# Kernel tuning notes

Hardware: AMD Instinct MI355X
Metric: run time of the kernel (lower is better)

The kernel has to match this reference:

```python
import jax, jax.numpy as jnp
import numpy as np
from jax.ops import segment_sum, segment_max

N_NODES = 100000
N_EDGES = 1600000
F_DIM = 64
N_GRAPHS = 64
K_HOPS = 3
EPS = 1e-5


def setup_inputs() -> dict:
    key = jax.random.key(0)
    ks = jax.random.split(key, 8)
    x = jax.random.normal(ks[0], (N_NODES, F_DIM), dtype=jnp.float32)
    edge_index = jax.random.randint(ks[1], (2, N_EDGES), 0, N_NODES, dtype=jnp.int32)
    batch = jnp.sort(jax.random.randint(ks[2], (N_NODES,), 0, N_GRAPHS, dtype=jnp.int32))
    edge_weight = jax.random.uniform(ks[3], (N_EDGES,), dtype=jnp.float32)
    # TAGConv params: K+1 hop-wise linear weights (no per-lin bias) + one output bias
    W = jax.random.normal(ks[4], (K_HOPS + 1, F_DIM, F_DIM), dtype=jnp.float32) * 0.05
    b = jnp.zeros((F_DIM,), dtype=jnp.float32)
    # GraphNorm params
    gn_weight = jnp.ones((F_DIM,), dtype=jnp.float32)
    gn_bias = jnp.zeros((F_DIM,), dtype=jnp.float32)
    gn_mean_scale = jnp.ones((F_DIM,), dtype=jnp.float32)
    return {"x": x, "edge_index": edge_index, "batch": batch, "edge_weight": edge_weight,
            "W": W, "b": b, "gn_weight": gn_weight, "gn_bias": gn_bias,
            "gn_mean_scale": gn_mean_scale}


def reference(x, edge_index, batch, edge_weight, W, b, gn_weight, gn_bias, gn_mean_scale):
    src, dst = edge_index[0], edge_index[1]

    # --- TAGConv: gcn_norm without self-loops ---
    deg = segment_sum(edge_weight, dst, num_segments=N_NODES)            # [N]
    dis = jnp.where(deg > 0, jax.lax.rsqrt(deg), 0.0)                    # deg^{-1/2}, inf -> 0
    norm = dis[src] * edge_weight * dis[dst]                             # [E]

    # out = sum_k (A_norm^k x) W_k + b
    out = x @ W[0]
    h = x
    for k in range(1, K_HOPS + 1):
        h = segment_sum(norm[:, None] * h[src], dst, num_segments=N_NODES)  # [N, F]
        out = out + h @ W[k]
    out = out + b

    # --- GraphNorm: per-graph mean/var with learnable mean_scale ---
    cnt = segment_sum(jnp.ones((N_NODES,), out.dtype), batch, num_segments=N_GRAPHS)
    cnt = jnp.maximum(cnt, 1.0)[:, None]                                  # [G, 1]
    mean = segment_sum(out, batch, num_segments=N_GRAPHS) / cnt          # [G, F]
    centered = out - mean[batch] * gn_mean_scale                         # [N, F]
    var = segment_sum(centered * centered, batch, num_segments=N_GRAPHS) / cnt
    hn = gn_weight * centered / jnp.sqrt(var + EPS)[batch] + gn_bias

    # --- residual + ReLU (add_residue=True) ---
    h_emb = jax.nn.relu(hn + x)                                          # [N, F]

    # --- global mean + max pooling ---
    mean_pool = segment_sum(h_emb, batch, num_segments=N_GRAPHS) / cnt   # [G, F]
    max_pool = segment_max(h_emb, batch, num_segments=N_GRAPHS)          # [G, F]
    flat = jnp.concatenate([mean_pool, max_pool], axis=-1)               # [G, 2F]

    return (h_emb, flat)
```

## Files before the change

kernel.cpp:

```cpp
#include <hip/hip_runtime.h>
#include <hip/hip_bf16.h>

#define NN 100000
#define NE 1600000
#define NG 64
#define FD 64
#define EPSV 1e-5f

typedef __hip_bfloat16 bf16;
typedef __attribute__((ext_vector_type(8))) short bf16x8;
typedef __attribute__((ext_vector_type(4))) float f32x4;

__device__ __forceinline__ float ldb(bf16 v) { return __bfloat162float(v); }
__device__ __forceinline__ bf16 f2b(float v) { return __float2bfloat16(v); }
__device__ __forceinline__ float b2f_bits(short s) {
    return __uint_as_float(((unsigned)(unsigned short)s) << 16);
}

#define NB1 391
#define CB 625
#define EPB 2560
#define CCN (NB1 * CB)
#define SCB2 ((CCN + 2047) / 2048)

__device__ __forceinline__ int xcd_chunk(int bid, int nwg) {
    int q = nwg >> 3, r = nwg & 7;
    int xcd = bid & 7, j = bid >> 3;
    return (xcd < r ? xcd * (q + 1) : r * (q + 1) + (xcd - r) * q) + j;
}

constexpr size_t ALGN(size_t x) { return (x + 255) & ~(size_t)255; }
constexpr size_t OFF_GSUM = 0;
constexpr size_t OFF_GSSQ = OFF_GSUM + ALGN((size_t)NG * FD * 4);
constexpr size_t OFF_GCNT = OFF_GSSQ + ALGN((size_t)NG * FD * 4);
constexpr size_t OFF_PSUM = OFF_GCNT + ALGN((size_t)NG * 4);
constexpr size_t OFF_PMAX = OFF_PSUM + ALGN((size_t)NG * FD * 4);
constexpr size_t ZERO_BYTES = OFF_PMAX + ALGN((size_t)NG * FD * 4);
constexpr size_t OFF_CNT  = ZERO_BYTES;
constexpr size_t OFF_DIS  = OFF_CNT  + ALGN((size_t)NN * 4);
constexpr size_t OFF_ROWP = OFF_DIS  + ALGN((size_t)NN * 4);
constexpr size_t OFF_BSUM = OFF_ROWP + ALGN((size_t)NN * 4);
constexpr size_t OFF_WT   = OFF_BSUM + ALGN(256 * 4);
constexpr size_t OFF_CSR  = OFF_WT   + ALGN(16384 * 2);
constexpr size_t OFF_H    = OFF_CSR  + ALGN((size_t)NE * 8);
constexpr size_t OFF_OUT  = OFF_H    + ALGN((size_t)NN * 256 * 2);
constexpr size_t OFF_CSRT = OFF_OUT;
constexpr size_t OFF_CC   = OFF_CSRT + ALGN((size_t)NE * 8);
static_assert(OFF_CC + (size_t)CCN * 4 - OFF_OUT <= (size_t)NN * FD * 4, "alias overflow");

#define XCB 25000
__global__ __launch_bounds__(256) void coarse_fused_kernel(const int* __restrict__ dst,
                                                           int* __restrict__ cc,
                                                           const float* __restrict__ x,
                                                           bf16* __restrict__ H,
                                                           const float* __restrict__ W,
                                                           bf16* __restrict__ Wt) {
    int b = blockIdx.x;
    if (b < CB) {
        __shared__ int hist[NB1];
        for (int i = threadIdx.x; i < NB1; i += 256) hist[i] = 0;
        __syncthreads();
        int e0 = b * EPB + threadIdx.x;
        #pragma unroll
        for (int i = 0; i < EPB / 256; i++)
            atomicAdd(&hist[dst[e0 + i * 256] >> 8], 1);
        __syncthreads();
        for (int i = threadIdx.x; i < NB1; i += 256)
            cc[(size_t)i * CB + b] = hist[i];
    } else if (b < CB + XCB) {
        int i = (b - CB) * 256 + threadIdx.x;
        if (i >= NN * 64) return;
        int node = i >> 6, f = i & 63;
        H[(size_t)node * 256 + f] = f2b(x[(size_t)node * 64 + f]);
    } else {
        int i = (b - CB - XCB) * 256 + threadIdx.x;
        int n = i & 63, kk = i >> 6;
        Wt[n * 256 + kk] = f2b(W[kk * 64 + n]);
    }
}

#define SCAN_BLK 256
#define SCAN_ITEMS 8
__global__ __launch_bounds__(SCAN_BLK) void scan_blocks(int* __restrict__ data,
                                                        int* __restrict__ bsum, int n) {
    __shared__ int lds[SCAN_BLK];
    int t = threadIdx.x, b = blockIdx.x;
    int base = b * SCAN_BLK * SCAN_ITEMS + t * SCAN_ITEMS;
    int v[SCAN_ITEMS];
    int s = 0;
    #pragma unroll
    for (int i = 0; i < SCAN_ITEMS; i++) {
        int idx = base + i;
        v[i] = (idx < n) ? data[idx] : 0;
        s += v[i];
    }
    lds[t] = s;
    __syncthreads();
    for (int off = 1; off < SCAN_BLK; off <<= 1) {
        int x = (t >= off) ? lds[t - off] : 0;
        __syncthreads();
        lds[t] += x;
        __syncthreads();
    }
    int excl = lds[t] - s;
    if (t == SCAN_BLK - 1) bsum[b] = lds[t];
    int run = excl;
    #pragma unroll
    for (int i = 0; i < SCAN_ITEMS; i++) {
        int idx = base + i;
        if (idx < n) data[idx] = run;
        run += v[i];
    }
}

__global__ __launch_bounds__(256) void bsum_scan(int* __restrict__ bsum, int nb) {
    __shared__ int lds[256];
    int t = threadIdx.x;
    int v = (t < nb) ? bsum[t] : 0;
    lds[t] = v;
    __syncthreads();
    for (int off = 1; off < 256; off <<= 1) {
        int x = (t >= off) ? lds[t - off] : 0;
        __syncthreads();
        lds[t] += x;
        __syncthreads();
    }
    if (t < nb) bsum[t] = lds[t] - v;
}

__global__ __launch_bounds__(256) void scan_add2(int* __restrict__ data,
                                                 const int* __restrict__ bpref, int n) {
    int i = blockIdx.x * 256 + threadIdx.x;
    if (i >= n) return;
    data[i] += bpref[i >> 11];
}

__global__ __launch_bounds__(256) void scatter2_kernel(const int* __restrict__ src,
                                                       const int* __restrict__ dst,
                                                       const float* __restrict__ ew,
                                                       const int* __restrict__ cc,
                                                       int2* __restrict__ csrt) {
    __shared__ int sc[512];
    __shared__ int gdel[NB1];
    __shared__ int2 stage[EPB];
    __shared__ int sdel[EPB];
    int t = threadIdx.x;
    int L = xcd_chunk(blockIdx.x, CB);

    sc[t] = 0; sc[t + 256] = 0;
    __syncthreads();

    int br[EPB / 256], px[EPB / 256], pw[EPB / 256];
    #pragma unroll
    for (int i = 0; i < EPB / 256; i++) {
        int e = L * EPB + i * 256 + t;
        int d = dst[e];
        int bk = d >> 8;
        int rk = atomicAdd(&sc[bk], 1);
        br[i] = bk | (rk << 9);
        px[i] = src[e] | ((d & 255) << 17);
        pw[i] = __float_as_int(ew[e]);
    }
    __syncthreads();

    for (int off = 1; off < 512; off <<= 1) {
        int a0 = (t >= off) ? sc[t - off] : 0;
        int a1 = sc[t + 256 - off];
        __syncthreads();
        sc[t] += a0; sc[t + 256] += a1;
        __syncthreads();
    }

    for (int i = t; i < NB1; i += 256)
        gdel[i] = cc[(size_t)i * CB + L] - ((i > 0) ? sc[i - 1] : 0);
    __syncthreads();

    #pragma unroll
    for (int i = 0; i < EPB / 256; i++) {
        int bk = br[i] & 511;
        int rk = br[i] >> 9;
        int slot = ((bk > 0) ? sc[bk - 1] : 0) + rk;
        stage[slot] = make_int2(px[i], pw[i]);
        sdel[slot] = gdel[bk];
    }
    __syncthreads();

    for (int j = t; j < EPB; j += 256)
        csrt[(size_t)(sdel[j] + j)] = stage[j];
}

__global__ __launch_bounds__(256) void fine_kernel(const int* __restrict__ cc,
                                                   const int2* __restrict__ csrt,
                                                   int2* __restrict__ csr,
                                                   int* __restrict__ rowp,
                                                   int* __restrict__ cnts,
                                                   float* __restrict__ dis) {
    __shared__ int hist[256];
    __shared__ float degw[256];
    __shared__ int pref[256];
    __shared__ int fcur[256];
    int b = blockIdx.x;
    int t = threadIdx.x;
    int base = cc[(size_t)b * CB];
    int end = (b == NB1 - 1) ? NE : cc[(size_t)(b + 1) * CB];
    int cnt = end - base;
    hist[t] = 0; degw[t] = 0.f;
    __syncthreads();
    for (int j = t; j < cnt; j += 256) {
        int2 e = csrt[base + j];
        int f = e.x >> 17;
        atomicAdd(&hist[f], 1);
        atomicAdd(&degw[f], __int_as_float(e.y));
    }
    __syncthreads();
    int hv = hist[t];
    pref[t] = hv;
    __syncthreads();
    for (int off = 1; off < 256; off <<= 1) {
        int x = (t >= off) ? pref[t - off] : 0;
        __syncthreads();
        pref[t] += x;
        __syncthreads();
    }
    int ex = pref[t] - hv;
    fcur[t] = ex;
    int node = b * 256 + t;
    if (node < NN) {
        rowp[node] = base + ex;
        cnts[node] = hv;
        float s = degw[t];
        dis[node] = (s > 0.f) ? rsqrtf(s) : 0.f;
    }
    __syncthreads();
    for (int j = t; j < cnt; j += 256) {
        int2 e = csrt[base + j];
        int f = e.x >> 17;
        int pos = atomicAdd(&fcur[f], 1);
        csr[base + pos] = make_int2(e.x & 0x1FFFF, e.y);
    }
}

template <bool FIRST>
__global__ __launch_bounds__(256) void hop_kernel(const bf16* __restrict__ hin,
                                                  bf16* __restrict__ hout,
                                                  const int* __restrict__ rowp,
                                                  const int* __restrict__ cnts,
                                                  int2* __restrict__ csr,
                                                  const float* __restrict__ dis) {
    int row = blockIdx.x * 4 + (threadIdx.x >> 6);
    if (row >= NN) return;
    row = __builtin_amdgcn_readfirstlane(row);
    int lane = threadIdx.x & 63;
    int sub = lane >> 3;
    int fl = lane & 7;
    int start = rowp[row];
    int cnt = cnts[row];
    float dr = dis[row];
    int2* cp = csr + start;

    float a[8] = {0, 0, 0, 0, 0, 0, 0, 0};

    if (cnt <= 24) {
        int2 e0 = (sub < cnt) ? cp[sub] : make_int2(0, 0);
        int2 e1 = (8 + sub < cnt) ? cp[8 + sub] : make_int2(0, 0);
        int2 e2 = (16 + sub < cnt) ? cp[16 + sub] : make_int2(0, 0);
        bf16x8 v0 = *(const bf16x8*)(hin + (size_t)e0.x * 256 + fl * 8);
        bf16x8 v1 = *(const bf16x8*)(hin + (size_t)e1.x * 256 + fl * 8);
        bf16x8 v2 = *(const bf16x8*)(hin + (size_t)e2.x * 256 + fl * 8);
        float w0 = __int_as_float(e0.y);
        float w1 = __int_as_float(e1.y);
        float w2 = __int_as_float(e2.y);
        if (FIRST) {
            w0 *= dis[e0.x]; w1 *= dis[e1.x]; w2 *= dis[e2.x];
            if (fl == 0) {
                if (sub < cnt)      cp[sub].y      = __float_as_int(w0);
                if (8 + sub < cnt)  cp[8 + sub].y  = __float_as_int(w1);
                if (16 + sub < cnt) cp[16 + sub].y = __float_as_int(w2);
            }
        }
        #pragma unroll
        for (int i = 0; i < 8; i++)
            a[i] = w0 * b2f_bits(v0[i]) + w1 * b2f_bits(v1[i]) + w2 * b2f_bits(v2[i]);
    } else {
        float b[8] = {0, 0, 0, 0, 0, 0, 0, 0};
        int j = 0;
        for (; j + 16 <= cnt; j += 16) {
            int2 e0 = cp[j + sub];
            int2 e1 = cp[j + 8 + sub];
            bf16x8 v0 = *(const bf16x8*)(hin + (size_t)e0.x * 256 + fl * 8);
            bf16x8 v1 = *(const bf16x8*)(hin + (size_t)e1.x * 256 + fl * 8);
            float w0 = __int_as_float(e0.y);
            float w1 = __int_as_float(e1.y);
            if (FIRST) {
                w0 *= dis[e0.x]; w1 *= dis[e1.x];
                if (fl == 0) {
                    cp[j + sub].y     = __float_as_int(w0);
                    cp[j + 8 + sub].y = __float_as_int(w1);
                }
            }
            #pragma unroll
            for (int i = 0; i < 8; i++) a[i] += w0 * b2f_bits(v0[i]);
            #pragma unroll
            for (int i = 0; i < 8; i++) b[i] += w1 * b2f_bits(v1[i]);
        }
        for (; j < cnt; j += 8) {
            int jj = j + sub;
            int2 e = (jj < cnt) ? cp[jj] : make_int2(0, 0);
            bf16x8 v = *(const bf16x8*)(hin + (size_t)e.x * 256 + fl * 8);
            float w = __int_as_float(e.y);
            if (FIRST) {
                w *= dis[e.x];
                if (fl == 0 && jj < cnt) cp[jj].y = __float_as_int(w);
            }
            #pragma unroll
            for (int i = 0; i < 8; i++) a[i] += w * b2f_bits(v[i]);
        }
        #pragma unroll
        for (int i = 0; i < 8; i++) a[i] += b[i];
    }

    #pragma unroll
    for (int i = 0; i < 8; i++) a[i] += __shfl_xor(a[i], 8);
    #pragma unroll
    for (int i = 0; i < 8; i++) a[i] += __shfl_xor(a[i], 16);
    #pragma unroll
    for (int i = 0; i < 8; i++) a[i] += __shfl_xor(a[i], 32);

    if (sub == 0) {
        bf16x8 ov;
        #pragma unroll
        for (int i = 0; i < 8; i++) {
            bf16 t = f2b(a[i] * dr);
            ov[i] = *(short*)&t;
        }
        *(bf16x8*)(hout + (size_t)row * 256 + fl * 8) = ov;
    }
}

#define GWAVES 1024
#define NT (NN / 16)

__global__ __launch_bounds__(256, 1) void gemm_kernel(const bf16* __restrict__ H,
                                                      const bf16* __restrict__ Wt,
                                                      const float* __restrict__ bias,
                                                      float* __restrict__ outb) {
    int wave = threadIdx.x >> 6;
    int lane = threadIdx.x & 63;
    int m = lane & 15, q = lane >> 4;
    int w = blockIdx.x * 4 + wave;

    bf16x8 B[4][8];
    #pragma unroll
    for (int n = 0; n < 4; n++) {
        const bf16* brow = Wt + (size_t)(n * 16 + m) * 256 + q * 8;
        #pragma unroll
        for (int ks = 0; ks < 8; ks++) B[n][ks] = *(const bf16x8*)(brow + ks * 32);
    }
    float bv[4];
    #pragma unroll
    for (int n = 0; n < 4; n++) bv[n] = bias[n * 16 + m];

    if (w >= NT) return;

    bf16x8 A0[8], A1[8];

    #define LOADA(dst_, t_)                                                  \
        {                                                                    \
            const bf16* arow = H + (size_t)((t_)*16 + m) * 256 + q * 8;      \
            _Pragma("unroll")                                                \
            for (int ks = 0; ks < 8; ks++)                                   \
                dst_[ks] = *(const bf16x8*)(arow + ks * 32);                 \
        }

    #define COMP(src_, t_)                                                   \
        {                                                                    \
            _Pragma("unroll")                                                \
            for (int n = 0; n < 4; n++) {                                    \
                f32x4 acc = {0.f, 0.f, 0.f, 0.f};                            \
                _Pragma("unroll")                                            \
                for (int ks = 0; ks < 8; ks++)                               \
                    acc = __builtin_amdgcn_mfma_f32_16x16x32_bf16(           \
                        src_[ks], B[n][ks], acc, 0, 0, 0);                   \
                _Pragma("unroll")                                            \
                for (int r = 0; r < 4; r++)                                  \
                    outb[(size_t)((t_)*16 + q * 4 + r) * 64 + n * 16 + m] =  \
                        acc[r] + bv[n];                                      \
            }                                                                \
        }

    int t = w;
    LOADA(A0, t)
    while (true) {
        int t1 = t + GWAVES;
        if (t1 < NT) LOADA(A1, t1)
        COMP(A0, t)
        if (t1 >= NT) return;
        int t2 = t1 + GWAVES;
        if (t2 < NT) LOADA(A0, t2)
        COMP(A1, t1)
        if (t2 >= NT) return;
        t = t2;
    }
    #undef LOADA
    #undef COMP
}

#define CH 32
#define STAT_WAVES ((NN + CH - 1) / CH)
#define STAT_BLOCKS ((STAT_WAVES * 64 + 255) / 256)

__global__ __launch_bounds__(256) void stats_kernel(const float* __restrict__ outb,
                                                    const int* __restrict__ batch,
                                                    float* __restrict__ gsum,
                                                    float* __restrict__ gssq,
                                                    float* __restrict__ gcnt) {
    int wid = (blockIdx.x * 256 + threadIdx.x) >> 6;
    int lane = threadIdx.x & 63;
    int n0 = wid * CH;
    if (n0 >= NN) return;
    int n1 = min(n0 + CH, NN);
    int g0 = batch[n0];
    if (n1 == n0 + CH && batch[n1 - 1] == g0) {
        float s = 0.f, s2 = 0.f;
        #pragma unroll
        for (int i = 0; i < CH; i++) {
            float v = outb[(size_t)(n0 + i) * 64 + lane];
            s += v; s2 += v * v;
        }
        atomicAdd(&gsum[g0 * 64 + lane], s);
        atomicAdd(&gssq[g0 * 64 + lane], s2);
        if (lane == 0) atomicAdd(&gcnt[g0], (float)CH);
    } else {
        int cur = g0; float s = 0.f, s2 = 0.f; int cl = 0;
        for (int i = n0; i < n1; i++) {
            int g = batch[i];
            if (g != cur) {
                atomicAdd(&gsum[cur * 64 + lane], s);
                atomicAdd(&gssq[cur * 64 + lane], s2);
                if (lane == 0) atomicAdd(&gcnt[cur], (float)cl);
                s = 0.f; s2 = 0.f; cl = 0; cur = g;
            }
            float v = outb[(size_t)i * 64 + lane];
            s += v; s2 += v * v; cl++;
        }
        atomicAdd(&gsum[cur * 64 + lane], s);
        atomicAdd(&gssq[cur * 64 + lane], s2);
        if (lane == 0) atomicAdd(&gcnt[cur], (float)cl);
    }
}

__device__ __forceinline__ void graph_mr(const float* gsum, const float* gssq,
                                         const float* gcnt, int g, int lane, float ms,
                                         float& mm, float& r) {
    float c = fmaxf(gcnt[g], 1.f);
    float mean = gsum[g * 64 + lane] / c;
    float msq = gssq[g * 64 + lane] / c;
    mm = mean * ms;
    float var = fmaxf(msq - 2.f * mm * mean + mm * mm, 0.f);
    r = rsqrtf(var + EPSV);
}

__global__ __launch_bounds__(256) void final_kernel(const float* __restrict__ outb,
                                                    const int* __restrict__ batch,
                                                    const float* __restrict__ xg,
                                                    const float* __restrict__ gsum,
                                                    const float* __restrict__ gssq,
                                                    const float* __restrict__ gcnt,
                                                    const float* __restrict__ gw_,
                                                    const float* __restrict__ gb_,
                                                    const float* __restrict__ ms_,
                                                    float* __restrict__ psum,
                                                    int* __restrict__ pmax,
                                                    float* __restrict__ hemb) {
    int wid = (blockIdx.x * 256 + threadIdx.x) >> 6;
    int lane = threadIdx.x & 63;
    int n0 = wid * CH;
    if (n0 >= NN) return;
    int n1 = min(n0 + CH, NN);
    float gw = gw_[lane], gb = gb_[lane], ms = ms_[lane];
    int g0 = batch[n0];
    if (n1 == n0 + CH && batch[n1 - 1] == g0) {
        float m, r;
        graph_mr(gsum, gssq, gcnt, g0, lane, ms, m, r);
        float ps = 0.f, pm = 0.f;
        #pragma unroll
        for (int i = 0; i < CH; i++) {
            size_t idx = (size_t)(n0 + i) * 64 + lane;
            float hn = gw * (outb[idx] - m) * r + gb;
            float he = hn + xg[idx];
            he = he > 0.f ? he : 0.f;
            hemb[idx] = he;
            ps += he;
            pm = fmaxf(pm, he);
        }
        atomicAdd(&psum[g0 * 64 + lane], ps);
        atomicMax(&pmax[g0 * 64 + lane], __float_as_int(pm));
    } else {
        int cur = g0;
        float m, r;
        graph_mr(gsum, gssq, gcnt, cur, lane, ms, m, r);
        float ps = 0.f, pm = 0.f;
        for (int i = n0; i < n1; i++) {
            int g = batch[i];
            if (g != cur) {
                atomicAdd(&psum[cur * 64 + lane], ps);
                atomicMax(&pmax[cur * 64 + lane], __float_as_int(pm));
                ps = 0.f; pm = 0.f; cur = g;
                graph_mr(gsum, gssq, gcnt, cur, lane, ms, m, r);
            }
            size_t idx = (size_t)i * 64 + lane;
            float hn = gw * (outb[idx] - m) * r + gb;
            float he = hn + xg[idx];
            he = he > 0.f ? he : 0.f;
            hemb[idx] = he;
            ps += he;
            pm = fmaxf(pm, he);
        }
        atomicAdd(&psum[cur * 64 + lane], ps);
        atomicMax(&pmax[cur * 64 + lane], __float_as_int(pm));
    }
}

__global__ __launch_bounds__(256) void pool_kernel(const float* __restrict__ psum,
                                                   const int* __restrict__ pmax,
                                                   const float* __restrict__ gcnt,
                                                   float* __restrict__ flat) {
    int i = blockIdx.x * 256 + threadIdx.x;
    if (i >= NG * FD) return;
    int g = i >> 6, f = i & 63;
    float c = fmaxf(gcnt[g], 1.f);
    flat[(size_t)g * 128 + f] = psum[i] / c;
    flat[(size_t)g * 128 + 64 + f] = __int_as_float(pmax[i]);
}

extern "C" void kernel_launch(void* const* d_in, const int* in_sizes, int n_in,
                              void* d_out, int out_size, void* d_ws, size_t ws_size,
                              hipStream_t stream) {
    const float* x = (const float*)d_in[0];
    const int* ei = (const int*)d_in[1];
    const int* batch = (const int*)d_in[2];
    const float* ew = (const float*)d_in[3];
    const float* W = (const float*)d_in[4];
    const float* bias = (const float*)d_in[5];
    const float* gnw = (const float*)d_in[6];
    const float* gnb = (const float*)d_in[7];
    const float* gms = (const float*)d_in[8];

    const int* src = ei;
    const int* dst = ei + NE;

    char* ws = (char*)d_ws;
    float* gsum = (float*)(ws + OFF_GSUM);
    float* gssq = (float*)(ws + OFF_GSSQ);
    float* gcnt = (float*)(ws + OFF_GCNT);
    float* psum = (float*)(ws + OFF_PSUM);
    int* pmax = (int*)(ws + OFF_PMAX);
    int* cnts = (int*)(ws + OFF_CNT);
    float* dis = (float*)(ws + OFF_DIS);
    int* rowp = (int*)(ws + OFF_ROWP);
    int* bsum = (int*)(ws + OFF_BSUM);
    bf16* Wt = (bf16*)(ws + OFF_WT);
    int2* csr = (int2*)(ws + OFF_CSR);
    bf16* H = (bf16*)(ws + OFF_H);
    float* outb = (float*)(ws + OFF_OUT);
    int2* csrt = (int2*)(ws + OFF_CSRT);
    int* cc = (int*)(ws + OFF_CC);

    float* hemb = (float*)d_out;
    float* flat = hemb + (size_t)NN * FD;

    hipMemsetAsync(d_ws, 0, ZERO_BYTES, stream);

    const int HOPB = (NN + 3) / 4;
    const int GFB = (NG * FD + 255) / 256;
    const int ADDB = (CCN + 255) / 256;

    coarse_fused_kernel<<<CB + XCB + 64, 256, 0, stream>>>(dst, cc, x, H, W, Wt);
    scan_blocks<<<SCB2, 256, 0, stream>>>(cc, bsum, CCN);
    bsum_scan<<<1, 256, 0, stream>>>(bsum, SCB2);
    scan_add2<<<ADDB, 256, 0, stream>>>(cc, bsum, CCN);
    scatter2_kernel<<<CB, 256, 0, stream>>>(src, dst, ew, cc, csrt);
    fine_kernel<<<NB1, 256, 0, stream>>>(cc, csrt, csr, rowp, cnts, dis);

    hop_kernel<true><<<HOPB, 256, 0, stream>>>(H, H + 64, rowp, cnts, csr, dis);
    hop_kernel<false><<<HOPB, 256, 0, stream>>>(H + 64, H + 128, rowp, cnts, csr, dis);
    hop_kernel<false><<<HOPB, 256, 0, stream>>>(H + 128, H + 192, rowp, cnts, csr, dis);

    gemm_kernel<<<GWAVES / 4, 256, 0, stream>>>(H, Wt, bias, outb);

    stats_kernel<<<STAT_BLOCKS, 256, 0, stream>>>(outb, batch, gsum, gssq, gcnt);
    final_kernel<<<STAT_BLOCKS, 256, 0, stream>>>(outb, batch, x, gsum, gssq, gcnt,
                                                  gnw, gnb, gms, psum, pmax, hemb);
    pool_kernel<<<GFB, 256, 0, stream>>>(psum, pmax, gcnt, flat);
}
```

Before: 353.5 us.

## Split hop features into planar per-hop arrays and process multiple rows per wave

```diff
diff --git a/kernel.cpp b/kernel.cpp
--- a/kernel.cpp
+++ b/kernel.cpp
@@ -48,7 +48,7 @@
 constexpr size_t OFF_CC   = OFF_CSRT + ALGN((size_t)NE * 8);
 static_assert(OFF_CC + (size_t)CCN * 4 - OFF_OUT <= (size_t)NN * FD * 4, "alias overflow");
 
-#define XCB 25000
+#define XCB 6250
 __global__ __launch_bounds__(256) void coarse_fused_kernel(const int* __restrict__ dst,
                                                            int* __restrict__ cc,
                                                            const float* __restrict__ x,
@@ -69,9 +69,12 @@
             cc[(size_t)i * CB + b] = hist[i];
     } else if (b < CB + XCB) {
         int i = (b - CB) * 256 + threadIdx.x;
-        if (i >= NN * 64) return;
-        int node = i >> 6, f = i & 63;
-        H[(size_t)node * 256 + f] = f2b(x[(size_t)node * 64 + f]);
+        float4 xv = ((const float4*)x)[i];
+        bf16 t0 = f2b(xv.x), t1 = f2b(xv.y), t2 = f2b(xv.z), t3 = f2b(xv.w);
+        ushort4 o;
+        o.x = *(unsigned short*)&t0; o.y = *(unsigned short*)&t1;
+        o.z = *(unsigned short*)&t2; o.w = *(unsigned short*)&t3;
+        ((ushort4*)H)[i] = o;
     } else {
         int i = (b - CB - XCB) * 256 + threadIdx.x;
         int n = i & 63, kk = i >> 6;
@@ -241,32 +244,17 @@
 }
 
 template <bool FIRST>
-__global__ __launch_bounds__(256) void hop_kernel(const bf16* __restrict__ hin,
-                                                  bf16* __restrict__ hout,
-                                                  const int* __restrict__ rowp,
-                                                  const int* __restrict__ cnts,
-                                                  int2* __restrict__ csr,
-                                                  const float* __restrict__ dis) {
-    int row = blockIdx.x * 4 + (threadIdx.x >> 6);
-    if (row >= NN) return;
-    row = __builtin_amdgcn_readfirstlane(row);
-    int lane = threadIdx.x & 63;
-    int sub = lane >> 3;
-    int fl = lane & 7;
-    int start = rowp[row];
-    int cnt = cnts[row];
-    float dr = dis[row];
-    int2* cp = csr + start;
-
-    float a[8] = {0, 0, 0, 0, 0, 0, 0, 0};
-
+__device__ __forceinline__ void row_accum_gen(const bf16* __restrict__ hin,
+                                              int2* cp, int cnt,
+                                              const float* __restrict__ dis,
+                                              int sub, int fl, float a[8]) {
     if (cnt <= 24) {
         int2 e0 = (sub < cnt) ? cp[sub] : make_int2(0, 0);
         int2 e1 = (8 + sub < cnt) ? cp[8 + sub] : make_int2(0, 0);
         int2 e2 = (16 + sub < cnt) ? cp[16 + sub] : make_int2(0, 0);
-        bf16x8 v0 = *(const bf16x8*)(hin + (size_t)e0.x * 256 + fl * 8);
-        bf16x8 v1 = *(const bf16x8*)(hin + (size_t)e1.x * 256 + fl * 8);
-        bf16x8 v2 = *(const bf16x8*)(hin + (size_t)e2.x * 256 + fl * 8);
+        bf16x8 v0 = *(const bf16x8*)(hin + (size_t)e0.x * 64 + fl * 8);
+        bf16x8 v1 = *(const bf16x8*)(hin + (size_t)e1.x * 64 + fl * 8);
+        bf16x8 v2 = *(const bf16x8*)(hin + (size_t)e2.x * 64 + fl * 8);
         float w0 = __int_as_float(e0.y);
         float w1 = __int_as_float(e1.y);
         float w2 = __int_as_float(e2.y);
@@ -280,15 +268,15 @@
         }
         #pragma unroll
         for (int i = 0; i < 8; i++)
-            a[i] = w0 * b2f_bits(v0[i]) + w1 * b2f_bits(v1[i]) + w2 * b2f_bits(v2[i]);
+            a[i] += w0 * b2f_bits(v0[i]) + w1 * b2f_bits(v1[i]) + w2 * b2f_bits(v2[i]);
     } else {
         float b[8] = {0, 0, 0, 0, 0, 0, 0, 0};
         int j = 0;
         for (; j + 16 <= cnt; j += 16) {
             int2 e0 = cp[j + sub];
             int2 e1 = cp[j + 8 + sub];
-            bf16x8 v0 = *(const bf16x8*)(hin + (size_t)e0.x * 256 + fl * 8);
-            bf16x8 v1 = *(const bf16x8*)(hin + (size_t)e1.x * 256 + fl * 8);
+            bf16x8 v0 = *(const bf16x8*)(hin + (size_t)e0.x * 64 + fl * 8);
+            bf16x8 v1 = *(const bf16x8*)(hin + (size_t)e1.x * 64 + fl * 8);
             float w0 = __int_as_float(e0.y);
             float w1 = __int_as_float(e1.y);
             if (FIRST) {
@@ -306,7 +294,7 @@
         for (; j < cnt; j += 8) {
             int jj = j + sub;
             int2 e = (jj < cnt) ? cp[jj] : make_int2(0, 0);
-            bf16x8 v = *(const bf16x8*)(hin + (size_t)e.x * 256 + fl * 8);
+            bf16x8 v = *(const bf16x8*)(hin + (size_t)e.x * 64 + fl * 8);
             float w = __int_as_float(e.y);
             if (FIRST) {
                 w *= dis[e.x];
@@ -318,22 +306,106 @@
         #pragma unroll
         for (int i = 0; i < 8; i++) a[i] += b[i];
     }
-
-    #pragma unroll
-    for (int i = 0; i < 8; i++) a[i] += __shfl_xor(a[i], 8);
-    #pragma unroll
-    for (int i = 0; i < 8; i++) a[i] += __shfl_xor(a[i], 16);
-    #pragma unroll
-    for (int i = 0; i < 8; i++) a[i] += __shfl_xor(a[i], 32);
+}
+
+template <bool FIRST, int R>
+__global__ __launch_bounds__(256) void hop_kernel(const bf16* __restrict__ hin,
+                                                  bf16* __restrict__ hout,
+                                                  const int* __restrict__ rowp,
+                                                  const int* __restrict__ cnts,
+                                                  int2* __restrict__ csr,
+                                                  const float* __restrict__ dis) {
+    int grp = blockIdx.x * 4 + (threadIdx.x >> 6);
+    int row0 = grp * R;
+    if (row0 >= NN) return;
+    row0 = __builtin_amdgcn_readfirstlane(row0);
+    int lane = threadIdx.x & 63;
+    int sub = lane >> 3;
+    int fl = lane & 7;
+
+    int cn[R]; float dr[R]; int2* cp[R];
+    bool fast = true;
+    #pragma unroll
+    for (int r = 0; r < R; r++) {
+        cp[r] = csr + rowp[row0 + r];
+        cn[r] = cnts[row0 + r];
+        dr[r] = dis[row0 + r];
+        fast = fast && (cn[r] <= 24);
+    }
+
+    float acc[R][8];
+    #pragma unroll
+    for (int r = 0; r < R; r++)
+        #pragma unroll
+        for (int i = 0; i < 8; i++) acc[r][i] = 0.f;
+
+    if (fast) {
+        int2 e[R][3];
+        #pragma unroll
+        for (int r = 0; r < R; r++)
+            #pragma unroll
+            for (int g = 0; g < 3; g++)
+                e[r][g] = (g * 8 + sub < cn[r]) ? cp[r][g * 8 + sub] : make_int2(0, 0);
+        bf16x8 v[R][3];
+        #pragma unroll
+        for (int r = 0; r < R; r++)
+            #pragma unroll
+            for (int g = 0; g < 3; g++)
+                v[r][g] = *(const bf16x8*)(hin + (size_t)e[r][g].x * 64 + fl * 8);
+        float w[R][3];
+        #pragma unroll
+        for (int r = 0; r < R; r++)
+            #pragma unroll
+            for (int g = 0; g < 3; g++)
+                w[r][g] = __int_as_float(e[r][g].y);
+        if (FIRST) {
+            #pragma unroll
+            for (int r = 0; r < R; r++)
+                #pragma unroll
+                for (int g = 0; g < 3; g++)
+                    w[r][g] *= dis[e[r][g].x];
+            if (fl == 0) {
+                #pragma unroll
+                for (int r = 0; r < R; r++)
+                    #pragma unroll
+                    for (int g = 0; g < 3; g++)
+                        if (g * 8 + sub < cn[r]) cp[r][g * 8 + sub].y = __float_as_int(w[r][g]);
+            }
+        }
+        #pragma unroll
+        for (int r = 0; r < R; r++)
+            #pragma unroll
+            for (int i = 0; i < 8; i++)
+                acc[r][i] = w[r][0] * b2f_bits(v[r][0][i])
+                          + w[r][1] * b2f_bits(v[r][1][i])
+                          + w[r][2] * b2f_bits(v[r][2][i]);
+    } else {
+        #pragma unroll
+        for (int r = 0; r < R; r++)
+            row_accum_gen<FIRST>(hin, cp[r], cn[r], dis, sub, fl, acc[r]);
+    }
+
+    #pragma unroll
+    for (int r = 0; r < R; r++) {
+        #pragma unroll
+        for (int i = 0; i < 8; i++) acc[r][i] += __shfl_xor(acc[r][i], 8);
+        #pragma unroll
+        for (int i = 0; i < 8; i++) acc[r][i] += __shfl_xor(acc[r][i], 16);
+        #pragma unroll
+        for (int i = 0; i < 8; i++) acc[r][i] += __shfl_xor(acc[r][i], 32);
+    }
 
     if (sub == 0) {
-        bf16x8 ov;
-        #pragma unroll
-        for (int i = 0; i < 8; i++) {
-            bf16 t = f2b(a[i] * dr);
-            ov[i] = *(short*)&t;
-        }
-        *(bf16x8*)(hout + (size_t)row * 256 + fl * 8) = ov;
+        #pragma unroll
+        for (int r = 0; r < R; r++) {
+            bf16x8 ov;
+            #pragma unroll
+            for (int i = 0; i < 8; i++) {
+                bf16 t = f2b(acc[r][i] * dr[r]);
+                ov[i] = *(short*)&t;
+            }
+            *(bf16x8*)(hout + (size_t)(row0 + r) * 64 + fl * 8) = ov;
+        }
     }
 }
 
@@ -364,12 +436,13 @@
 
     bf16x8 A0[8], A1[8];
 
-    #define LOADA(dst_, t_)                                                  \
-        {                                                                    \
-            const bf16* arow = H + (size_t)((t_)*16 + m) * 256 + q * 8;      \
-            _Pragma("unroll")                                                \
-            for (int ks = 0; ks < 8; ks++)                                   \
-                dst_[ks] = *(const bf16x8*)(arow + ks * 32);                 \
+    #define LOADA(dst_, t_)                                                      \
+        {                                                                        \
+            _Pragma("unroll")                                                    \
+            for (int ks = 0; ks < 8; ks++)                                       \
+                dst_[ks] = *(const bf16x8*)(H +                                  \
+                    ((size_t)(ks >> 1) * NN + (size_t)((t_)*16 + m)) * 64 +      \
+                    (ks & 1) * 32 + q * 8);                                      \
         }
 
     #define COMP(src_, t_)                                                   \
@@ -571,7 +644,9 @@
 
     hipMemsetAsync(d_ws, 0, ZERO_BYTES, stream);
 
-    const int HOPB = (NN + 3) / 4;
+    const size_t PL = (size_t)NN * 64;
+    const int HOPB2 = (NN / 2 + 3) / 4;
+    const int HOPB4 = (NN / 4 + 3) / 4;
     const int GFB = (NG * FD + 255) / 256;
     const int ADDB = (CCN + 255) / 256;
 
@@ -582,9 +657,9 @@
     scatter2_kernel<<<CB, 256, 0, stream>>>(src, dst, ew, cc, csrt);
     fine_kernel<<<NB1, 256, 0, stream>>>(cc, csrt, csr, rowp, cnts, dis);
 
-    hop_kernel<true><<<HOPB, 256, 0, stream>>>(H, H + 64, rowp, cnts, csr, dis);
-    hop_kernel<false><<<HOPB, 256, 0, stream>>>(H + 64, H + 128, rowp, cnts, csr, dis);
-    hop_kernel<false><<<HOPB, 256, 0, stream>>>(H + 128, H + 192, rowp, cnts, csr, dis);
+    hop_kernel<true, 2><<<HOPB2, 256, 0, stream>>>(H, H + PL, rowp, cnts, csr, dis);
+    hop_kernel<false, 4><<<HOPB4, 256, 0, stream>>>(H + PL, H + 2 * PL, rowp, cnts, csr, dis);
+    hop_kernel<false, 4><<<HOPB4, 256, 0, stream>>>(H + 2 * PL, H + 3 * PL, rowp, cnts, csr, dis);
 
     gemm_kernel<<<GWAVES / 4, 256, 0, stream>>>(H, Wt, bias, outb);
 
```

Result: no change. 350.9 us (-0.7%).
